# Kernel tuning notes

Hardware: AMD Instinct MI355X
Metric: run time of the kernel (lower is better)

The kernel has to match this reference:

```python
import jax, jax.numpy as jnp
import numpy as np

N_NODES = 10000
N_EDGES = 160000
IN_C = 32
OUT_C = 32
FC = 32
DIM = 3
RADIUS = 1.0
LN_EPS = 1e-5


def _layernorm(x, g, b):
    mu = jnp.mean(x, axis=-1, keepdims=True)
    var = jnp.mean(jnp.square(x - mu), axis=-1, keepdims=True)
    return (x - mu) * jax.lax.rsqrt(var + LN_EPS) * g + b


def setup_inputs() -> dict:
    key = jax.random.key(0)
    ks = jax.random.split(key, 10)
    inp = {
        "features": jax.random.normal(ks[0], (N_NODES, IN_C), dtype=jnp.float32),
        "hood_coords": jax.random.normal(ks[1], (N_EDGES, DIM), dtype=jnp.float32),
        "source": jax.random.randint(ks[2], (N_EDGES,), 0, N_NODES, dtype=jnp.int32),
        "target": jax.random.randint(ks[3], (N_EDGES,), 0, N_NODES, dtype=jnp.int32),
        # neural field params: Linear(DIM,FC) -> LN -> ReLU -> Linear(FC,FC) -> LN -> ReLU -> Linear(FC, IN_C*OUT_C) -> Tanh
        "W0": jax.random.normal(ks[4], (DIM, FC), dtype=jnp.float32) * 0.3,
        "b0": jnp.zeros((FC,), dtype=jnp.float32),
        "g0": jnp.ones((FC,), dtype=jnp.float32),
        "beta0": jnp.zeros((FC,), dtype=jnp.float32),
        "W1": jax.random.normal(ks[5], (FC, FC), dtype=jnp.float32) * 0.15,
        "b1": jnp.zeros((FC,), dtype=jnp.float32),
        "g1": jnp.ones((FC,), dtype=jnp.float32),
        "beta1": jnp.zeros((FC,), dtype=jnp.float32),
        "W2": jax.random.normal(ks[6], (FC, IN_C * OUT_C), dtype=jnp.float32) * 0.15,
        "b2": jnp.zeros((IN_C * OUT_C,), dtype=jnp.float32),
    }
    return inp


def reference(features, hood_coords, source, target,
              W0, b0, g0, beta0, W1, b1, g1, beta1, W2, b2):
    m = features.shape[0]
    # neural field: per-edge weight matrix w [E, OUT_C, IN_C]
    x = hood_coords / RADIUS
    h = jax.nn.relu(_layernorm(x @ W0 + b0, g0, beta0))
    h = jax.nn.relu(_layernorm(h @ W1 + b1, g1, beta1))
    w = jnp.tanh(h @ W2 + b2).reshape(-1, OUT_C, IN_C)
    # gather + batched matvec: out[e,o] = sum_i f[e,i] * w[e,o,i]
    f = features[source]
    oc = jnp.einsum('ni,noi->no', f, w)
    # scatter_mean over target nodes
    sums = jax.ops.segment_sum(oc, target, num_segments=m)
    counts = jax.ops.segment_sum(jnp.ones((target.shape[0],), dtype=oc.dtype),
                                 target, num_segments=m)
    counts = jnp.maximum(counts, 1.0)
    return sums / counts[:, None]
```

## Files before the change

### kernel.cpp

```cpp
#include <hip/hip_runtime.h>

#define LN_EPS 1e-5f

typedef __attribute__((ext_vector_type(8)))  short short8;
typedef __attribute__((ext_vector_type(4)))  short short4v;
typedef __attribute__((ext_vector_type(4)))  float floatx4;
typedef __attribute__((ext_vector_type(16))) float floatx16;

__device__ __forceinline__ unsigned short f2bf(float x) {
    unsigned u = __float_as_uint(x);
    u += 0x7FFFu + ((u >> 16) & 1u);
    return (unsigned short)(u >> 16);
}

__global__ __launch_bounds__(256) void k_edge_mlp(
    const float* __restrict__ coords,
    const int*   __restrict__ target,
    const float* __restrict__ W0, const float* __restrict__ b0,
    const float* __restrict__ g0, const float* __restrict__ be0,
    const float* __restrict__ W1, const float* __restrict__ b1,
    const float* __restrict__ g1, const float* __restrict__ be1,
    const float* __restrict__ W2, unsigned short* __restrict__ w2frag,
    unsigned short* __restrict__ hfrag, int* __restrict__ counts,
    int* __restrict__ rank, int E, int nEB)
{
    const int tid = threadIdx.x;

    if (blockIdx.x >= nEB) {
        const int idx = (blockIdx.x - nEB) * 256 + tid;
        if (idx < 4096) {
            const int l  = idx & 63;
            const int ot = idx >> 6;
            const int t  = ot & 1;
            const int o  = ot >> 1;
            const int row = l & 31;
            const int kb  = t*16 + (l >> 5)*8;
            short8 v;
            #pragma unroll
            for (int b = 0; b < 8; ++b)
                v[b] = (short)f2bf(W2[(size_t)(kb + b)*1024 + o*32 + row]);
            ((short8*)w2frag)[idx] = v;
        }
        return;
    }

    __shared__ float sW0[3*32], sW1T[32*36];
    __shared__ float sb0[32], sg0[32], sbe0[32], sb1[32], sg1[32], sbe1[32];
    for (int i = tid; i < 32*32; i += 256) {
        const int o = i & 31, c = i >> 5;
        sW1T[o*36 + c] = W1[i];
    }
    if (tid < 96) sW0[tid] = W0[tid];
    if (tid < 32) {
        sb0[tid] = b0[tid];  sg0[tid] = g0[tid];  sbe0[tid] = be0[tid];
        sb1[tid] = b1[tid];  sg1[tid] = g1[tid];  sbe1[tid] = be1[tid];
    }
    __syncthreads();

    const int e = blockIdx.x * 256 + tid;
    if (e >= E) return;

    const float x0 = coords[e*3+0];
    const float x1 = coords[e*3+1];
    const float x2 = coords[e*3+2];

    float h[32];
    #pragma unroll
    for (int o = 0; o < 32; ++o)
        h[o] = x0*sW0[o] + x1*sW0[32+o] + x2*sW0[64+o] + sb0[o];

    {
        float mu = 0.f;
        #pragma unroll
        for (int o = 0; o < 32; ++o) mu += h[o];
        mu *= (1.f/32.f);
        float var = 0.f;
        #pragma unroll
        for (int o = 0; o < 32; ++o) { float d = h[o]-mu; var += d*d; }
        var *= (1.f/32.f);
        const float inv = rsqrtf(var + LN_EPS);
        #pragma unroll
        for (int o = 0; o < 32; ++o)
            h[o] = fmaxf((h[o]-mu)*inv*sg0[o] + sbe0[o], 0.f);
    }

    float h2[32];
    #pragma unroll
    for (int o = 0; o < 32; ++o) {
        float s = sb1[o];
        #pragma unroll
        for (int c4 = 0; c4 < 8; ++c4) {
            const floatx4 wv = *reinterpret_cast<const floatx4*>(&sW1T[o*36 + c4*4]);
            s += h[c4*4+0]*wv[0] + h[c4*4+1]*wv[1]
               + h[c4*4+2]*wv[2] + h[c4*4+3]*wv[3];
        }
        h2[o] = s;
    }

    {
        float mu = 0.f;
        #pragma unroll
        for (int o = 0; o < 32; ++o) mu += h2[o];
        mu *= (1.f/32.f);
        float var = 0.f;
        #pragma unroll
        for (int o = 0; o < 32; ++o) { float d = h2[o]-mu; var += d*d; }
        var *= (1.f/32.f);
        const float inv = rsqrtf(var + LN_EPS);
        #pragma unroll
        for (int o = 0; o < 32; ++o)
            h2[o] = fmaxf((h2[o]-mu)*inv*sg1[o] + sbe1[o], 0.f);
    }

    const int et = e >> 5, er = e & 31;
    short8* base = (short8*)(hfrag) + (size_t)et * 128;
    #pragma unroll
    for (int t = 0; t < 2; ++t) {
        #pragma unroll
        for (int kg = 0; kg < 2; ++kg) {
            short8 v;
            #pragma unroll
            for (int b = 0; b < 8; ++b) v[b] = (short)f2bf(h2[t*16 + kg*8 + b]);
            base[t*64 + kg*32 + er] = v;
        }
    }

    rank[e] = atomicAdd(&counts[target[e]], 1);
}

__global__ __launch_bounds__(1024) void k_scan(
    const int* __restrict__ counts, int* __restrict__ offs, int N)
{
    __shared__ int wsum[16];
    const int t = threadIdx.x;
    const int lane = t & 63, w = t >> 6;
    const int CH = (N + 1023) >> 10;
    const int beg = t * CH;

    int s = 0;
    for (int k = 0; k < CH; ++k) {
        const int i = beg + k;
        if (i < N) s += counts[i];
    }
    int incl = s;
    #pragma unroll
    for (int d = 1; d < 64; d <<= 1) {
        const int x = __shfl_up(incl, d);
        if (lane >= d) incl += x;
    }
    if (lane == 63) wsum[w] = incl;
    __syncthreads();
    if (t == 0) {
        int run = 0;
        #pragma unroll
        for (int i = 0; i < 16; ++i) { const int v = wsum[i]; wsum[i] = run; run += v; }
    }
    __syncthreads();
    const int base = wsum[w] + incl - s;
    int run = base;
    for (int k = 0; k < CH; ++k) {
        const int i = beg + k;
        if (i < N) { offs[i] = run; run += counts[i]; }
    }
    if (t == 1023) offs[N] = base + s;
}

__global__ __launch_bounds__(256, 2) void k_field_mfma(
    const unsigned short* __restrict__ hfrag,
    const unsigned short* __restrict__ w2frag,
    const float* __restrict__ features,
    const int*   __restrict__ src,
    const int*   __restrict__ tgt,
    const int*   __restrict__ rank,
    const int*   __restrict__ offs,
    const float* __restrict__ b2,
    unsigned short* __restrict__ ocP,
    int netiles)
{
    __shared__ float s_b2s[1024];
    const int tid = threadIdx.x;
    const float KE = 2.8853900817779268f;
    #pragma unroll
    for (int r = 0; r < 4; ++r) s_b2s[tid + 256*r] = KE * b2[tid + 256*r];

    const int lane = tid & 63;
    const int wq   = tid >> 6;
    const int jh   = blockIdx.x & 1;
    const int W    = jh*4 + wq;
    const int h5   = lane >> 5;
    const int ecol = lane & 31;
    const float* b2base = &s_b2s[W*128 + 4*h5];

    short8 afr[8];
    #pragma unroll
    for (int u = 0; u < 8; ++u)
        afr[u] = ((const short8*)w2frag)[(W*8 + u)*64 + lane];
    __syncthreads();

    const floatx16 z16 = {0.f,0.f,0.f,0.f,0.f,0.f,0.f,0.f,
                          0.f,0.f,0.f,0.f,0.f,0.f,0.f,0.f};

    const int nunits = 2*netiles;
    for (int unit = blockIdx.x; unit < nunits; unit += gridDim.x) {
        const int et = unit >> 1;
        const int e0 = et << 5;
        const short8 bs0 = ((const short8*)hfrag)[et*128 + lane];
        const short8 bs1 = ((const short8*)hfrag)[et*128 + 64 + lane];

        const int sN = src[e0 + ecol];
        const int p  = offs[tgt[e0 + ecol]] + rank[e0 + ecol];

        floatx4 fv[4];
        float fsl = 0.f;
        #pragma unroll
        for (int rq = 0; rq < 4; ++rq) {
            fv[rq] = *reinterpret_cast<const floatx4*>(
                         features + (size_t)sN*32 + rq*8 + 4*h5);
            #pragma unroll
            for (int rr = 0; rr < 4; ++rr) fsl += fv[rq][rr];
        }

        float q[4];
        #pragma unroll
        for (int u = 0; u < 4; ++u) {
            floatx16 d = __builtin_amdgcn_mfma_f32_32x32x16_bf16(afr[2*u],   bs0, z16, 0, 0, 0);
            d          = __builtin_amdgcn_mfma_f32_32x32x16_bf16(afr[2*u+1], bs1, d,   0, 0, 0);
            float sf0 = 0.f, sf1 = 0.f, sf2 = 0.f, sf3 = 0.f;
            #pragma unroll
            for (int qq = 0; qq < 4; ++qq) {
                const floatx4 bq = *reinterpret_cast<const floatx4*>(b2base + u*32 + 8*qq);
                const float t0 = fmaf(d[qq*4+0], KE, bq[0]);
                sf0 = fmaf(fv[qq][0], __builtin_amdgcn_rcpf(__builtin_amdgcn_exp2f(t0) + 1.0f), sf0);
                const float t1 = fmaf(d[qq*4+1], KE, bq[1]);
                sf1 = fmaf(fv[qq][1], __builtin_amdgcn_rcpf(__builtin_amdgcn_exp2f(t1) + 1.0f), sf1);
                const float t2 = fmaf(d[qq*4+2], KE, bq[2]);
                sf2 = fmaf(fv[qq][2], __builtin_amdgcn_rcpf(__builtin_amdgcn_exp2f(t2) + 1.0f), sf2);
                const float t3 = fmaf(d[qq*4+3], KE, bq[3]);
                sf3 = fmaf(fv[qq][3], __builtin_amdgcn_rcpf(__builtin_amdgcn_exp2f(t3) + 1.0f), sf3);
            }
            const float sf = (sf0 + sf1) + (sf2 + sf3);
            const float v  = fmaf(-2.0f, sf, fsl);
            q[u] = v + __shfl_xor(v, 32);
        }

        if (lane < 32) {
            short4v vv;
            #pragma unroll
            for (int u = 0; u < 4; ++u) vv[u] = (short)f2bf(q[u]);
            *reinterpret_cast<short4v*>(ocP + (size_t)p*32 + W*4) = vv;
        }
    }
}

__global__ __launch_bounds__(256) void k_gather(
    const unsigned short* __restrict__ ocP,
    const int* __restrict__ offs,
    float* __restrict__ out, int N)
{
    const int node = blockIdx.x * 4 + (threadIdx.x >> 6);
    const int lane = threadIdx.x & 63;
    if (node >= N) return;
    const int r = lane >> 3;
    const int c = lane & 7;
    const int beg = offs[node], end = offs[node + 1];

    float a0 = 0.f, a1 = 0.f, a2 = 0.f, a3 = 0.f;
    for (int k = beg + r; k < end; k += 8) {
        const uint2 v = *reinterpret_cast<const uint2*>(ocP + (size_t)k*32 + c*4);
        a0 += __uint_as_float(v.x << 16);
        a1 += __uint_as_float(v.x & 0xFFFF0000u);
        a2 += __uint_as_float(v.y << 16);
        a3 += __uint_as_float(v.y & 0xFFFF0000u);
    }
    #pragma unroll
    for (int m = 8; m < 64; m <<= 1) {
        a0 += __shfl_xor(a0, m);
        a1 += __shfl_xor(a1, m);
        a2 += __shfl_xor(a2, m);
        a3 += __shfl_xor(a3, m);
    }
    if (lane < 8) {
        const float rinv = __builtin_amdgcn_rcpf(fmaxf((float)(end - beg), 1.0f));
        floatx4 o4 = {a0*rinv, a1*rinv, a2*rinv, a3*rinv};
        *reinterpret_cast<floatx4*>(out + (size_t)node*32 + lane*4) = o4;
    }
}

extern "C" void kernel_launch(void* const* d_in, const int* in_sizes, int n_in,
                              void* d_out, int out_size, void* d_ws, size_t ws_size,
                              hipStream_t stream)
{
    const float* features = (const float*)d_in[0];
    const float* coords   = (const float*)d_in[1];
    const int*   src      = (const int*)  d_in[2];
    const int*   tgt      = (const int*)  d_in[3];
    const float* W0  = (const float*)d_in[4];
    const float* b0  = (const float*)d_in[5];
    const float* g0  = (const float*)d_in[6];
    const float* be0 = (const float*)d_in[7];
    const float* W1  = (const float*)d_in[8];
    const float* b1  = (const float*)d_in[9];
    const float* g1  = (const float*)d_in[10];
    const float* be1 = (const float*)d_in[11];
    const float* W2  = (const float*)d_in[12];
    const float* b2  = (const float*)d_in[13];

    const int E = in_sizes[2];
    const int N = in_sizes[0] / 32;

    char* p = (char*)d_ws;
    unsigned short* hfrag  = (unsigned short*)p;  p += (size_t)E*32*2;
    unsigned short* ocP    = (unsigned short*)p;  p += (size_t)E*32*2;
    unsigned short* w2frag = (unsigned short*)p;  p += 32*1024*2;
    int* rankArr = (int*)p;  p += (size_t)E*4;
    int* counts  = (int*)p;  p += (size_t)N*4;
    int* offs    = (int*)p;  p += (size_t)(N+1)*4;

    (void)hipMemsetAsync(counts, 0, (size_t)N*4, stream);

    const int nEB = (E + 255)/256;
    k_edge_mlp<<<nEB + 16, 256, 0, stream>>>(
        coords, tgt, W0, b0, g0, be0, W1, b1, g1, be1, W2, w2frag,
        hfrag, counts, rankArr, E, nEB);

    k_scan<<<1, 1024, 0, stream>>>(counts, offs, N);

    const int netiles = E / 32;
    k_field_mfma<<<2048, 256, 0, stream>>>(
        hfrag, w2frag, features, src, tgt, rankArr, offs, b2, ocP, netiles);

    k_gather<<<(N + 3)/4, 256, 0, stream>>>(ocP, offs, (float*)d_out, N);
}
```

Before: 115.2 us.

## Switch field kernel to 16x16x32 MFMA tiles with LDS-staged output

Replaces the 32x32x16 MFMA formulation with 16x16x32 MFMA over 16-edge tiles, where each wave handles one output channel and each block covers four channels. The w2/h fragment layouts change to match. Per-wave register use drops sharply (two A fragments instead of eight), so launch bounds go up to 4 blocks per SM for higher occupancy. In exchange, each output row now goes through a shared-memory staging buffer with a block-wide barrier every iteration, and the work is split into eight times as many units.

```diff
diff --git a/kernel.cpp b/kernel.cpp
--- a/kernel.cpp
+++ b/kernel.cpp
@@ -3,9 +3,7 @@
 #define LN_EPS 1e-5f
 
 typedef __attribute__((ext_vector_type(8)))  short short8;
-typedef __attribute__((ext_vector_type(4)))  short short4v;
 typedef __attribute__((ext_vector_type(4)))  float floatx4;
-typedef __attribute__((ext_vector_type(16))) float floatx16;
 
 __device__ __forceinline__ unsigned short f2bf(float x) {
     unsigned u = __float_as_uint(x);
@@ -30,15 +28,13 @@
         const int idx = (blockIdx.x - nEB) * 256 + tid;
         if (idx < 4096) {
             const int l  = idx & 63;
-            const int ot = idx >> 6;
-            const int t  = ot & 1;
-            const int o  = ot >> 1;
-            const int row = l & 31;
-            const int kb  = t*16 + (l >> 5)*8;
+            const int jt = idx >> 6;
+            const int j  = jt*16 + (l & 15);
+            const int kb = (l >> 4) * 8;
             short8 v;
             #pragma unroll
             for (int b = 0; b < 8; ++b)
-                v[b] = (short)f2bf(W2[(size_t)(kb + b)*1024 + o*32 + row]);
+                v[b] = (short)f2bf(W2[(size_t)(kb + b)*1024 + j]);
             ((short8*)w2frag)[idx] = v;
         }
         return;
@@ -112,17 +108,14 @@
             h2[o] = fmaxf((h2[o]-mu)*inv*sg1[o] + sbe1[o], 0.f);
     }
 
-    const int et = e >> 5, er = e & 31;
-    short8* base = (short8*)(hfrag) + (size_t)et * 128;
-    #pragma unroll
-    for (int t = 0; t < 2; ++t) {
-        #pragma unroll
-        for (int kg = 0; kg < 2; ++kg) {
-            short8 v;
-            #pragma unroll
-            for (int b = 0; b < 8; ++b) v[b] = (short)f2bf(h2[t*16 + kg*8 + b]);
-            base[t*64 + kg*32 + er] = v;
-        }
+    const int et = e >> 4, er = e & 15;
+    short8* base = (short8*)(hfrag) + (size_t)et * 64;
+    #pragma unroll
+    for (int kg = 0; kg < 4; ++kg) {
+        short8 v;
+        #pragma unroll
+        for (int b = 0; b < 8; ++b) v[b] = (short)f2bf(h2[kg*8 + b]);
+        base[er + 16*kg] = v;
     }
 
     rank[e] = atomicAdd(&counts[target[e]], 1);
@@ -165,7 +158,7 @@
     if (t == 1023) offs[N] = base + s;
 }
 
-__global__ __launch_bounds__(256, 2) void k_field_mfma(
+__global__ __launch_bounds__(256, 4) void k_field_mfma(
     const unsigned short* __restrict__ hfrag,
     const unsigned short* __restrict__ w2frag,
     const float* __restrict__ features,
@@ -177,77 +170,68 @@
     unsigned short* __restrict__ ocP,
     int netiles)
 {
-    __shared__ float s_b2s[1024];
-    const int tid = threadIdx.x;
-    const float KE = 2.8853900817779268f;
-    #pragma unroll
-    for (int r = 0; r < 4; ++r) s_b2s[tid + 256*r] = KE * b2[tid + 256*r];
-
+    __shared__ unsigned short sOC[2][16][4];
+    __shared__ int sP[2][16];
+    const int tid  = threadIdx.x;
     const int lane = tid & 63;
     const int wq   = tid >> 6;
-    const int jh   = blockIdx.x & 1;
-    const int W    = jh*4 + wq;
-    const int h5   = lane >> 5;
-    const int ecol = lane & 31;
-    const float* b2base = &s_b2s[W*128 + 4*h5];
-
-    short8 afr[8];
-    #pragma unroll
-    for (int u = 0; u < 8; ++u)
-        afr[u] = ((const short8*)w2frag)[(W*8 + u)*64 + lane];
-    __syncthreads();
-
-    const floatx16 z16 = {0.f,0.f,0.f,0.f,0.f,0.f,0.f,0.f,
-                          0.f,0.f,0.f,0.f,0.f,0.f,0.f,0.f};
-
-    const int nunits = 2*netiles;
-    for (int unit = blockIdx.x; unit < nunits; unit += gridDim.x) {
-        const int et = unit >> 1;
-        const int e0 = et << 5;
-        const short8 bs0 = ((const short8*)hfrag)[et*128 + lane];
-        const short8 bs1 = ((const short8*)hfrag)[et*128 + 64 + lane];
+    const int oq   = blockIdx.x & 7;
+    const int o    = oq*4 + wq;
+    const int g    = lane >> 4;
+    const int ecol = lane & 15;
+    const float KE = 2.8853900817779268f;
+
+    const short8 afr0 = ((const short8*)w2frag)[(o*2    )*64 + lane];
+    const short8 afr1 = ((const short8*)w2frag)[(o*2 + 1)*64 + lane];
+
+    floatx4 b2v0, b2v1;
+    {
+        const floatx4 t0 = *reinterpret_cast<const floatx4*>(b2 + o*32 + g*4);
+        const floatx4 t1 = *reinterpret_cast<const floatx4*>(b2 + o*32 + 16 + g*4);
+        #pragma unroll
+        for (int r = 0; r < 4; ++r) { b2v0[r] = KE*t0[r]; b2v1[r] = KE*t1[r]; }
+    }
+
+    const floatx4 z4 = {0.f, 0.f, 0.f, 0.f};
+    const int nunits = 8*netiles;
+    int buf = 0;
+    for (int unit = blockIdx.x; unit < nunits; unit += gridDim.x, buf ^= 1) {
+        const int et = unit >> 3;
+        const int e0 = et << 4;
+        const short8 bs = ((const short8*)hfrag)[et*64 + lane];
 
         const int sN = src[e0 + ecol];
         const int p  = offs[tgt[e0 + ecol]] + rank[e0 + ecol];
-
-        floatx4 fv[4];
-        float fsl = 0.f;
-        #pragma unroll
-        for (int rq = 0; rq < 4; ++rq) {
-            fv[rq] = *reinterpret_cast<const floatx4*>(
-                         features + (size_t)sN*32 + rq*8 + 4*h5);
-            #pragma unroll
-            for (int rr = 0; rr < 4; ++rr) fsl += fv[rq][rr];
+        if (tid < 16) sP[buf][tid] = p;
+
+        const floatx4 fv0 = *reinterpret_cast<const floatx4*>(
+                                features + (size_t)sN*32 + g*4);
+        const floatx4 fv1 = *reinterpret_cast<const floatx4*>(
+                                features + (size_t)sN*32 + 16 + g*4);
+        const float fsl = ((fv0[0]+fv0[1]) + (fv0[2]+fv0[3]))
+                        + ((fv1[0]+fv1[1]) + (fv1[2]+fv1[3]));
+
+        const floatx4 d0 = __builtin_amdgcn_mfma_f32_16x16x32_bf16(afr0, bs, z4, 0, 0, 0);
+        const floatx4 d1 = __builtin_amdgcn_mfma_f32_16x16x32_bf16(afr1, bs, z4, 0, 0, 0);
+
+        float sf0 = 0.f, sf1 = 0.f;
+        #pragma unroll
+        for (int r = 0; r < 4; ++r) {
+            const float t0 = fmaf(d0[r], KE, b2v0[r]);
+            sf0 = fmaf(fv0[r], __builtin_amdgcn_rcpf(__builtin_amdgcn_exp2f(t0) + 1.0f), sf0);
+            const float t1 = fmaf(d1[r], KE, b2v1[r]);
+            sf1 = fmaf(fv1[r], __builtin_amdgcn_rcpf(__builtin_amdgcn_exp2f(t1) + 1.0f), sf1);
         }
-
-        float q[4];
-        #pragma unroll
-        for (int u = 0; u < 4; ++u) {
-            floatx16 d = __builtin_amdgcn_mfma_f32_32x32x16_bf16(afr[2*u],   bs0, z16, 0, 0, 0);
-            d          = __builtin_amdgcn_mfma_f32_32x32x16_bf16(afr[2*u+1], bs1, d,   0, 0, 0);
-            float sf0 = 0.f, sf1 = 0.f, sf2 = 0.f, sf3 = 0.f;
-            #pragma unroll
-            for (int qq = 0; qq < 4; ++qq) {
-                const floatx4 bq = *reinterpret_cast<const floatx4*>(b2base + u*32 + 8*qq);
-                const float t0 = fmaf(d[qq*4+0], KE, bq[0]);
-                sf0 = fmaf(fv[qq][0], __builtin_amdgcn_rcpf(__builtin_amdgcn_exp2f(t0) + 1.0f), sf0);
-                const float t1 = fmaf(d[qq*4+1], KE, bq[1]);
-                sf1 = fmaf(fv[qq][1], __builtin_amdgcn_rcpf(__builtin_amdgcn_exp2f(t1) + 1.0f), sf1);
-                const float t2 = fmaf(d[qq*4+2], KE, bq[2]);
-                sf2 = fmaf(fv[qq][2], __builtin_amdgcn_rcpf(__builtin_amdgcn_exp2f(t2) + 1.0f), sf2);
-                const float t3 = fmaf(d[qq*4+3], KE, bq[3]);
-                sf3 = fmaf(fv[qq][3], __builtin_amdgcn_rcpf(__builtin_amdgcn_exp2f(t3) + 1.0f), sf3);
-            }
-            const float sf = (sf0 + sf1) + (sf2 + sf3);
-            const float v  = fmaf(-2.0f, sf, fsl);
-            q[u] = v + __shfl_xor(v, 32);
-        }
-
-        if (lane < 32) {
-            short4v vv;
-            #pragma unroll
-            for (int u = 0; u < 4; ++u) vv[u] = (short)f2bf(q[u]);
-            *reinterpret_cast<short4v*>(ocP + (size_t)p*32 + W*4) = vv;
+        float v = fmaf(-2.0f, sf0 + sf1, fsl);
+        v += __shfl_xor(v, 16);
+        v += __shfl_xor(v, 32);
+
+        if (lane < 16) sOC[buf][ecol][wq] = f2bf(v);
+        __syncthreads();
+        if (tid < 32) {
+            const int row = tid >> 1, half = tid & 1;
+            const unsigned val = ((const unsigned*)&sOC[buf][row][0])[half];
+            ((unsigned*)ocP)[(size_t)sP[buf][row]*16 + oq*2 + half] = val;
         }
     }
 }
@@ -325,7 +309,7 @@
 
     k_scan<<<1, 1024, 0, stream>>>(counts, offs, N);
 
-    const int netiles = E / 32;
+    const int netiles = E / 16;
     k_field_mfma<<<2048, 256, 0, stream>>>(
         hfrag, w2frag, features, src, tgt, rankArr, offs, b2, ocP, netiles);
 
```

Measured after the change: 148.9 us. 1.29x slower.

## Process two edge tiles per iteration and stage outputs in LDS for coalesced stores

Applied to the files above, without the earlier changes.

Each block now handles two edge-tile units per loop iteration, issuing both tiles' loads up front so more memory latency is in flight. The per-wave scattered 8-byte bf16 stores are replaced by staging results in a padded, double-buffered shared-memory tile. After a block barrier, each row's 16-byte half is written with contiguous 8-byte stores. This adds a __syncthreads per iteration and raises register pressure from the doubled fragments. It also contains an odd `FV*0.f` term that could block fast-math folding.

```diff
diff --git a/kernel.cpp b/kernel.cpp
--- a/kernel.cpp
+++ b/kernel.cpp
@@ -3,7 +3,6 @@
 #define LN_EPS 1e-5f
 
 typedef __attribute__((ext_vector_type(8)))  short short8;
-typedef __attribute__((ext_vector_type(4)))  short short4v;
 typedef __attribute__((ext_vector_type(4)))  float floatx4;
 typedef __attribute__((ext_vector_type(16))) float floatx16;
 
@@ -165,6 +164,31 @@
     if (t == 1023) offs[N] = base + s;
 }
 
+#define FIELD_COMPUTE(BS0, BS1, FV, FSL, QOUT)                                 \
+    {                                                                          \
+        _Pragma("unroll")                                                      \
+        for (int u = 0; u < 4; ++u) {                                          \
+            floatx16 d = __builtin_amdgcn_mfma_f32_32x32x16_bf16(afr[2*u],   (BS0), z16, 0, 0, 0); \
+            d          = __builtin_amdgcn_mfma_f32_32x32x16_bf16(afr[2*u+1], (BS1), d,   0, 0, 0); \
+            float sf0 = 0.f, sf1 = 0.f, sf2 = 0.f, sf3 = 0.f;                  \
+            _Pragma("unroll")                                                  \
+            for (int qq = 0; qq < 4; ++qq) {                                   \
+                const floatx4 bq = *reinterpret_cast<const floatx4*>(b2base + u*32 + 8*qq); \
+                const float t0 = fmaf((FV)[qq][0]*0.f + d[qq*4+0], KE, bq[0]); \
+                sf0 = fmaf((FV)[qq][0], __builtin_amdgcn_rcpf(__builtin_amdgcn_exp2f(t0) + 1.0f), sf0); \
+                const float t1 = fmaf(d[qq*4+1], KE, bq[1]);                   \
+                sf1 = fmaf((FV)[qq][1], __builtin_amdgcn_rcpf(__builtin_amdgcn_exp2f(t1) + 1.0f), sf1); \
+                const float t2 = fmaf(d[qq*4+2], KE, bq[2]);                   \
+                sf2 = fmaf((FV)[qq][2], __builtin_amdgcn_rcpf(__builtin_amdgcn_exp2f(t2) + 1.0f), sf2); \
+                const float t3 = fmaf(d[qq*4+3], KE, bq[3]);                   \
+                sf3 = fmaf((FV)[qq][3], __builtin_amdgcn_rcpf(__builtin_amdgcn_exp2f(t3) + 1.0f), sf3); \
+            }                                                                  \
+            const float sf = (sf0 + sf1) + (sf2 + sf3);                        \
+            const float v  = fmaf(-2.0f, sf, (FSL));                           \
+            (QOUT)[u] = v + __shfl_xor(v, 32);                                 \
+        }                                                                      \
+    }
+
 __global__ __launch_bounds__(256, 2) void k_field_mfma(
     const unsigned short* __restrict__ hfrag,
     const unsigned short* __restrict__ w2frag,
@@ -178,6 +202,8 @@
     int netiles)
 {
     __shared__ float s_b2s[1024];
+    __shared__ unsigned int sOC[2][2][32*9];
+    __shared__ int sP[2][64];
     const int tid = threadIdx.x;
     const float KE = 2.8853900817779268f;
     #pragma unroll
@@ -190,6 +216,8 @@
     const int h5   = lane >> 5;
     const int ecol = lane & 31;
     const float* b2base = &s_b2s[W*128 + 4*h5];
+    const int str = tid >> 2;
+    const int sti = (tid & 3) * 2;
 
     short8 afr[8];
     #pragma unroll
@@ -201,53 +229,62 @@
                           0.f,0.f,0.f,0.f,0.f,0.f,0.f,0.f};
 
     const int nunits = 2*netiles;
-    for (int unit = blockIdx.x; unit < nunits; unit += gridDim.x) {
-        const int et = unit >> 1;
-        const int e0 = et << 5;
-        const short8 bs0 = ((const short8*)hfrag)[et*128 + lane];
-        const short8 bs1 = ((const short8*)hfrag)[et*128 + 64 + lane];
-
-        const int sN = src[e0 + ecol];
-        const int p  = offs[tgt[e0 + ecol]] + rank[e0 + ecol];
-
-        floatx4 fv[4];
-        float fsl = 0.f;
+    const int g = gridDim.x;
+    int buf = 0;
+    for (int unit = blockIdx.x; unit < nunits; unit += 2*g, buf ^= 1) {
+        const int unitB = unit + g;
+        const bool hasB = (unitB < nunits);
+        const int etA = unit >> 1;
+        const int e0A = etA << 5;
+        const int etB = (hasB ? unitB : unit) >> 1;
+        const int e0B = etB << 5;
+
+        const short8 bsA0 = ((const short8*)hfrag)[etA*128 + lane];
+        const short8 bsA1 = ((const short8*)hfrag)[etA*128 + 64 + lane];
+        const short8 bsB0 = ((const short8*)hfrag)[etB*128 + lane];
+        const short8 bsB1 = ((const short8*)hfrag)[etB*128 + 64 + lane];
+        const int sNA = src[e0A + ecol];
+        const int sNB = src[e0B + ecol];
+        if (tid < 32) {
+            sP[buf][ecol]      = offs[tgt[e0A + ecol]] + rank[e0A + ecol];
+            sP[buf][32 + ecol] = offs[tgt[e0B + ecol]] + rank[e0B + ecol];
+        }
+
+        floatx4 fvA[4], fvB[4];
+        float fslA = 0.f, fslB = 0.f;
         #pragma unroll
         for (int rq = 0; rq < 4; ++rq) {
-            fv[rq] = *reinterpret_cast<const floatx4*>(
-                         features + (size_t)sN*32 + rq*8 + 4*h5);
+            fvA[rq] = *reinterpret_cast<const floatx4*>(
+                          features + (size_t)sNA*32 + rq*8 + 4*h5);
+            fvB[rq] = *reinterpret_cast<const floatx4*>(
+                          features + (size_t)sNB*32 + rq*8 + 4*h5);
             #pragma unroll
-            for (int rr = 0; rr < 4; ++rr) fsl += fv[rq][rr];
-        }
-
-        float q[4];
-        #pragma unroll
-        for (int u = 0; u < 4; ++u) {
-            floatx16 d = __builtin_amdgcn_mfma_f32_32x32x16_bf16(afr[2*u],   bs0, z16, 0, 0, 0);
-            d          = __builtin_amdgcn_mfma_f32_32x32x16_bf16(afr[2*u+1], bs1, d,   0, 0, 0);
-            float sf0 = 0.f, sf1 = 0.f, sf2 = 0.f, sf3 = 0.f;
-            #pragma unroll
-            for (int qq = 0; qq < 4; ++qq) {
-                const floatx4 bq = *reinterpret_cast<const floatx4*>(b2base + u*32 + 8*qq);
-                const float t0 = fmaf(d[qq*4+0], KE, bq[0]);
-                sf0 = fmaf(fv[qq][0], __builtin_amdgcn_rcpf(__builtin_amdgcn_exp2f(t0) + 1.0f), sf0);
-                const float t1 = fmaf(d[qq*4+1], KE, bq[1]);
-                sf1 = fmaf(fv[qq][1], __builtin_amdgcn_rcpf(__builtin_amdgcn_exp2f(t1) + 1.0f), sf1);
-                const float t2 = fmaf(d[qq*4+2], KE, bq[2]);
-                sf2 = fmaf(fv[qq][2], __builtin_amdgcn_rcpf(__builtin_amdgcn_exp2f(t2) + 1.0f), sf2);
-                const float t3 = fmaf(d[qq*4+3], KE, bq[3]);
-                sf3 = fmaf(fv[qq][3], __builtin_amdgcn_rcpf(__builtin_amdgcn_exp2f(t3) + 1.0f), sf3);
+            for (int rr = 0; rr < 4; ++rr) {
+                fslA += fvA[rq][rr];
+                fslB += fvB[rq][rr];
             }
-            const float sf = (sf0 + sf1) + (sf2 + sf3);
-            const float v  = fmaf(-2.0f, sf, fsl);
-            q[u] = v + __shfl_xor(v, 32);
-        }
+        }
+
+        float qA[4], qB[4];
+        FIELD_COMPUTE(bsA0, bsA1, fvA, fslA, qA);
+        FIELD_COMPUTE(bsB0, bsB1, fvB, fslB, qB);
 
         if (lane < 32) {
-            short4v vv;
-            #pragma unroll
-            for (int u = 0; u < 4; ++u) vv[u] = (short)f2bf(q[u]);
-            *reinterpret_cast<short4v*>(ocP + (size_t)p*32 + W*4) = vv;
+            sOC[buf][0][ecol*9 + wq*2]     = ((unsigned)f2bf(qA[1]) << 16) | f2bf(qA[0]);
+            sOC[buf][0][ecol*9 + wq*2 + 1] = ((unsigned)f2bf(qA[3]) << 16) | f2bf(qA[2]);
+            sOC[buf][1][ecol*9 + wq*2]     = ((unsigned)f2bf(qB[1]) << 16) | f2bf(qB[0]);
+            sOC[buf][1][ecol*9 + wq*2 + 1] = ((unsigned)f2bf(qB[3]) << 16) | f2bf(qB[2]);
+        }
+        __syncthreads();
+        {
+            const int uh = str >> 5, r32 = str & 31;
+            if (uh == 0 || hasB) {
+                const unsigned v0 = sOC[buf][uh][r32*9 + sti];
+                const unsigned v1 = sOC[buf][uh][r32*9 + sti + 1];
+                unsigned* dst = (unsigned*)ocP + (size_t)sP[buf][str]*16 + jh*8 + sti;
+                dst[0] = v0;
+                dst[1] = v1;
+            }
         }
     }
 }
```

After: 159.3 us. 38.2% more time.
